# Kernel tuning notes

Measured on AMD Instinct MI355X. Metric: run time of the kernel, lower is better.

Reference implementation:

```python
import jax, jax.numpy as jnp
import numpy as np

B, L, K = 16, 512, 30          # proteins, residues per protein, kNN neighbors
N = B * L
H, FC = 32, 3                  # h_channels, frame_channels
C = H + FC                     # fused sphere channels (35)
HEADS, AC, VC = 8, 16, 8       # heads, alpha channels (H//2), value channels (H//4)
RBF_N, POS_N = 16, 16
EF = RBF_N + POS_N

# idealized backbone atom positions (N, CA, C) in the local residue frame
IDEAL_BB = np.array([[-0.525, 1.363, 0.0], [0.0, 0.0, 0.0], [1.526, 0.0, 0.0]], dtype=np.float32)
# cartesian (x,y,z) -> real-SH l=1 ordering (y,z,x)
P_SH = np.array([[0., 1., 0.], [0., 0., 1.], [1., 0., 0.]], dtype=np.float32)


def _knn_edges(trans):
    # per-chain brute-force kNN (chains are contiguous blocks of length L)
    X = trans.reshape(B, L, 3)
    d2 = jnp.sum((X[:, :, None, :] - X[:, None, :, :]) ** 2, axis=-1)  # [B,L,L]
    d2 = d2 + jnp.eye(L, dtype=d2.dtype) * 1e9                          # exclude self
    _, idx = jax.lax.top_k(-d2, K)                                      # [B,L,K]
    off = (jnp.arange(B) * L)[:, None, None]
    src = (idx + off).reshape(-1)              # neighbor (edge_index[0])
    tgt = jnp.repeat(jnp.arange(N), K)         # center   (edge_index[1])
    return src, tgt


def _edge_rot_mat(vec):
    # rotation aligning the edge vector with the y axis (eSCN init_edge_rot_mat style)
    nx = vec / (jnp.linalg.norm(vec, axis=-1, keepdims=True) + 1e-12)
    ref = jnp.where(jnp.abs(nx[:, :1]) < 0.9,
                    jnp.array([1., 0., 0.], dtype=vec.dtype),
                    jnp.array([0., 0., 1.], dtype=vec.dtype))
    nz = jnp.cross(nx, ref)
    nz = nz / (jnp.linalg.norm(nz, axis=-1, keepdims=True) + 1e-12)
    ny = jnp.cross(nx, nz)
    ny = ny / (jnp.linalg.norm(ny, axis=-1, keepdims=True) + 1e-12)
    return jnp.stack([nz, nx, ny], axis=-2)  # [E,3,3]


def _rbf(d, d_min=0.0, d_max=20.0, count=RBF_N):
    mu = jnp.linspace(d_min, d_max, count)
    sigma = (d_max - d_min) / count
    return jnp.exp(-(((d[:, None] - mu) / sigma) ** 2))


def _pos_emb(src, tgt, num=POS_N):
    d = (src - tgt).astype(jnp.float32)
    freq = jnp.exp(jnp.arange(0, num, 2, dtype=jnp.float32) * (-np.log(10000.0) / num))
    ang = d[:, None] * freq
    return jnp.concatenate([jnp.cos(ang), jnp.sin(ang)], axis=-1)


def _forward(rots, trans, node_emb, batch, x_mask, noising_mask,
             W_alpha, a_vec, W_v, W_o, W_g, W_2):
    src, tgt = _knn_edges(trans)
    vec = trans[src] - trans[tgt]
    dist = jnp.linalg.norm(vec, axis=-1)
    valid = jnp.isfinite(dist) & (dist > 1e-3)  # edge_select, applied as mask

    R = _edge_rot_mat(vec)
    P = jnp.asarray(P_SH)
    D1 = jnp.einsum('ij,ejk,lk->eil', P, R, P)  # l=1 Wigner in real-SH basis [E,3,3]

    edge_features = jnp.concatenate([_rbf(dist), _pos_emb(src, tgt)], axis=-1)  # [E,32]

    # fuse node features with backbone frame atoms and editability flag
    frame_atoms = jnp.einsum('nij,aj->nai', rots, jnp.asarray(IDEAL_BB))  # [N,3atoms,3xyz]
    editable = noising_mask & (~x_mask)
    emb = jnp.zeros((N, 4, C), dtype=node_emb.dtype)
    emb = emb.at[:, :, :H].set(node_emb)
    emb = emb.at[:, 1:4, H:].set(jnp.swapaxes(frame_atoms, -1, -2))
    emb = emb.at[:, 0, C - 1].set(editable.astype(node_emb.dtype))

    # gather + rotate source features into edge frames
    xs = emb[src]                                                   # [E,4,C]
    xs_rot = jnp.concatenate([xs[:, :1], jnp.einsum('eij,ejc->eic', D1, xs[:, 1:])], axis=1)

    # invariant attention logits (l=0 of rotated src, l=0 of tgt, edge feats)
    inv = jnp.concatenate([xs_rot[:, 0], emb[tgt, 0], edge_features], axis=-1)  # [E,102]
    hdn = jax.nn.silu(inv @ W_alpha).reshape(-1, HEADS, AC)
    logits = jax.nn.leaky_relu(jnp.einsum('ehk,hk->eh', hdn, a_vec), 0.2)
    logits = jnp.where(valid[:, None], logits, -1e9)

    # segment softmax over incoming edges of each target node
    mx = jax.lax.stop_gradient(jax.ops.segment_max(logits, tgt, num_segments=N))
    ex = jnp.exp(logits - mx[tgt]) * valid[:, None].astype(logits.dtype)
    den = jax.ops.segment_sum(ex, tgt, num_segments=N)
    alpha = ex / (den[tgt] + 1e-9)                                  # [E,HEADS]

    # equivariant values, attention-weighted, rotate back, scatter
    v = (xs_rot @ W_v).reshape(-1, 4, HEADS, VC)
    m = (v * alpha[:, None, :, None]).reshape(-1, 4, HEADS * VC)
    m = jnp.concatenate([m[:, :1], jnp.einsum('eji,ejc->eic', D1, m[:, 1:])], axis=1)  # D^T
    agg = jax.ops.segment_sum(m, tgt, num_segments=N)               # [N,4,64]

    y = agg @ W_o                                                    # [N,4,H]
    gate = jax.nn.silu(y[:, 0] @ W_g)                                # invariant gating FFN
    return (y * gate[:, None, :]) @ W_2                              # [N,4,H]


def setup_inputs():
    key = jax.random.key(0)
    ks = jax.random.split(key, 12)
    rots = jax.vmap(lambda m: jnp.linalg.qr(m)[0])(jax.random.normal(ks[0], (N, 3, 3)))
    trans = jax.random.normal(ks[1], (N, 3)) * 10.0
    node_emb = jax.random.normal(ks[2], (N, 4, H))
    batch = jnp.repeat(jnp.arange(B, dtype=jnp.int32), L)
    x_mask = jax.random.randint(ks[3], (N,), 0, 2).astype(bool)
    noising_mask = jax.random.randint(ks[4], (N,), 0, 2).astype(bool)
    s = lambda k, sh, fan: jax.random.normal(k, sh) / np.sqrt(fan)
    return dict(rots=rots, trans=trans, node_emb=node_emb, batch=batch,
                x_mask=x_mask, noising_mask=noising_mask,
                W_alpha=s(ks[5], (2 * C + EF, HEADS * AC), 2 * C + EF),
                a_vec=s(ks[6], (HEADS, AC), AC),
                W_v=s(ks[7], (C, HEADS * VC), C),
                W_o=s(ks[8], (HEADS * VC, H), HEADS * VC),
                W_g=s(ks[9], (H, H), H),
                W_2=s(ks[10], (H, H), H))


def reference(rots, trans, node_emb, batch, x_mask, noising_mask,
              W_alpha, a_vec, W_v, W_o, W_g, W_2):
    return _forward(rots, trans, node_emb, batch, x_mask, noising_mask,
                    W_alpha, a_vec, W_v, W_o, W_g, W_2)
```

## Files before the change

kernel.cpp:

```cpp
#include <hip/hip_runtime.h>
#include <cstdint>

#define B_ 16
#define L_ 512
#define N_ 8192
#define K_ 30
#define E_ (N_*K_)
#define H_ 32
#define C_ 35

typedef uint16_t u16;
typedef uint32_t u32;
typedef unsigned long long u64;
typedef float f2v __attribute__((ext_vector_type(2)));

static __device__ __forceinline__ f2v splat2(float x) { f2v v; v.x = x; v.y = x; return v; }

static __device__ __forceinline__ float ldf(const void* p, int i, int bf) {
    return bf ? __uint_as_float(((u32)((const u16*)p)[i]) << 16)
              : ((const float*)p)[i];
}
static __device__ __forceinline__ float bfu16(u16 x) {
    return __uint_as_float(((u32)x) << 16);
}
static __device__ __forceinline__ int ldmask(const void* p, int i, int mode) {
    if (mode == 0) return ((const unsigned char*)p)[i] != 0;
    if (mode == 2) return ((const u32*)p)[2*i] != 0;
    return ((const u32*)p)[i] != 0;
}
static __device__ __forceinline__ u16 f2bf(float f) {
    u32 x = __float_as_uint(f);
    u32 r = x + 0x7FFFu + ((x >> 16) & 1u);
    return (u16)(r >> 16);
}
static __device__ __forceinline__ float fsilu(float x) {
    return x * __builtin_amdgcn_rcpf(1.f + __expf(-x));
}

static __device__ __forceinline__ int detect_bf(const void* tr, int lane) {
    const u16* p = (const u16*)tr;
    int cnt = 0;
    for (int i = lane; i < 256; i += 64) {
        u16 v = p[2 * i];
        int e = (v >> 7) & 0xFF;
        if ((e >= 100 && e <= 141) || (v & 0x7FFFu) == 0) cnt++;
    }
    #pragma unroll
    for (int d = 1; d < 64; d <<= 1) cnt += __shfl_xor(cnt, d, 64);
    return cnt >= 192;
}
static __device__ __forceinline__ int detect_mm(const void* xmv, int lane) {
    const u32* xm = (const u32*)xmv;
    int anyBig = 0, oddNZ = 0;
    for (int i = lane; i < 1024; i += 64) {
        u32 w = xm[i];
        if (w & ~1u) anyBig = 1;
        if ((i & 1) && w) oddNZ = 1;
    }
    #pragma unroll
    for (int d = 1; d < 64; d <<= 1) {
        anyBig |= __shfl_xor(anyBig, d, 64);
        oddNZ  |= __shfl_xor(oddNZ, d, 64);
    }
    return anyBig ? 0 : (oddNZ ? 1 : 2);
}

__constant__ float cBB[9] = {-0.525f, 1.363f, 0.f,  0.f, 0.f, 0.f,  1.526f, 0.f, 0.f};

#define DPP_UMIN(var, CTRL) \
    { u32 o_ = (u32)__builtin_amdgcn_update_dpp((int)(var), (int)(var), CTRL, 0xF, 0xF, false); \
      (var) = (o_ < (var)) ? o_ : (var); }
#define DPP_UMIN_ALL(var) \
    DPP_UMIN(var, 0x111) DPP_UMIN(var, 0x112) DPP_UMIN(var, 0x114) \
    DPP_UMIN(var, 0x118) DPP_UMIN(var, 0x142) DPP_UMIN(var, 0x143)

#define DPP_ADD8(part) \
    part += __uint_as_float((u32)__builtin_amdgcn_update_dpp( \
        (int)__float_as_uint(part), (int)__float_as_uint(part), 0xB1, 0xF, 0xF, false)); \
    part += __uint_as_float((u32)__builtin_amdgcn_update_dpp( \
        (int)__float_as_uint(part), (int)__float_as_uint(part), 0x4E, 0xF, 0xF, false)); \
    part += __uint_as_float((u32)__builtin_amdgcn_update_dpp( \
        (int)__float_as_uint(part), (int)__float_as_uint(part), 0x141, 0xF, 0xF, false));

__global__ __launch_bounds__(256) void mega_kernel(
    const void* __restrict__ rots, const void* __restrict__ trans,
    const void* __restrict__ node, const void* __restrict__ xm,
    const void* __restrict__ nm,
    const void* __restrict__ Wa, const void* __restrict__ av,
    const void* __restrict__ Wv, const void* __restrict__ Wo,
    const void* __restrict__ Wg, const void* __restrict__ W2,
    int* __restrict__ flag, int* __restrict__ srcArr,
    float* __restrict__ hsrc, float* __restrict__ htgt,
    float* __restrict__ ptab, float* __restrict__ V,
    float* __restrict__ c_wrb, float* __restrict__ c_av,
    float* __restrict__ c_Wo, float* __restrict__ c_Wg, float* __restrict__ c_W2)
{
    __shared__ float sX[L_], sY[L_], sZ[L_];
    __shared__ float eS[140];
    __shared__ int flagS[2];
    const int bid = blockIdx.x, tid = threadIdx.x;
    const int lane = tid & 63, wid = tid >> 6;

    if (bid < 2048) {
        if (wid == 0) {
            int bf = detect_bf(trans, lane);
            if (lane == 0) flagS[0] = bf;
        }
        __syncthreads();
        const int bf = flagS[0];
        const int t0 = bid * 4;
        const int base = (t0 >> 9) << 9;
        if (bf) {
            const u16* tp = (const u16*)trans;
            for (int i = tid; i < L_; i += 256) {
                sX[i] = bfu16(tp[(base + i) * 3 + 0]);
                sY[i] = bfu16(tp[(base + i) * 3 + 1]);
                sZ[i] = bfu16(tp[(base + i) * 3 + 2]);
            }
        } else {
            const float* tp = (const float*)trans;
            for (int i = tid; i < L_; i += 256) {
                sX[i] = tp[(base + i) * 3 + 0];
                sY[i] = tp[(base + i) * 3 + 1];
                sZ[i] = tp[(base + i) * 3 + 2];
            }
        }
        __syncthreads();

        const int t = t0 + wid;
        const int l = t & 511;
        const float tx = sX[l], ty = sY[l], tz = sZ[l];

        u32 d2b[8];
        #pragma unroll
        for (int i = 0; i < 8; ++i) {
            int j = lane + (i << 6);
            float dx = __fsub_rn(tx, sX[j]);
            float dy = __fsub_rn(ty, sY[j]);
            float dz = __fsub_rn(tz, sZ[j]);
            float d2 = __fadd_rn(__fadd_rn(__fmul_rn(dx, dx), __fmul_rn(dy, dy)), __fmul_rn(dz, dz));
            if (j == l) d2 = __fadd_rn(d2, 1e9f);
            d2b[i] = __float_as_uint(d2);
        }

        int myres = 0;
        for (int k = 0; k < K_; ++k) {
            u32 bb = d2b[0]; int bs = 0;
            #pragma unroll
            for (int i = 1; i < 8; ++i)
                if (d2b[i] < bb) { bb = d2b[i]; bs = i; }
            u32 m = bb;
            DPP_UMIN_ALL(m)
            u32 gbits = (u32)__builtin_amdgcn_readlane((int)m, 63);
            u32 cand = (bb == gbits) ? (u32)(lane | (bs << 6)) : 0xFFFFFFFFu;
            DPP_UMIN_ALL(cand)
            u32 gidx = (u32)__builtin_amdgcn_readlane((int)cand, 63);
            if (lane == (u32)k) myres = (int)(gidx & 511u);
            if ((gidx & 63u) == (u32)lane) {
                int ws = (int)(gidx >> 6);
                #pragma unroll
                for (int i = 0; i < 8; ++i)
                    if (ws == i) d2b[i] = 0xFFFFFFFFu;
            }
        }
        if (lane < K_) srcArr[t * K_ + lane] = base + myres;

    } else if (bid < 10240) {
        const int n = bid - 2048;
        if (wid == 0) {
            int bf = detect_bf(trans, lane);
            int mm = detect_mm(xm, lane);
            if (lane == 0) { flagS[0] = bf; flagS[1] = mm; }
        }
        __syncthreads();
        const int bf = flagS[0], mm = flagS[1];
        if (tid < 140) {
            int r = tid / 35, c = tid - r * 35;
            float v;
            if (c < H_) {
                v = ldf(node, n * 128 + r * 32 + c, bf);
            } else if (r == 0) {
                v = (c == 34) ? ((ldmask(nm, n, mm) && !ldmask(xm, n, mm)) ? 1.f : 0.f) : 0.f;
            } else {
                int i = r - 1, a = c - 32;
                v = ldf(rots, n*9 + i*3 + 0, bf) * cBB[a*3 + 0]
                  + ldf(rots, n*9 + i*3 + 1, bf) * cBB[a*3 + 1]
                  + ldf(rots, n*9 + i*3 + 2, bf) * cBB[a*3 + 2];
            }
            eS[tid] = v;
        }
        __syncthreads();
        const int r = tid >> 6, cc = tid & 63;
        if (bf) {
            const u16* wa = (const u16*)Wa;
            const u16* wv = (const u16*)Wv;
            if (tid < 128) {
                float a = 0.f, b = 0.f;
                #pragma unroll 5
                for (int i = 0; i < 35; ++i) {
                    float v = eS[i];
                    a = fmaf(v, bfu16(wa[i * 128 + tid]),        a);
                    b = fmaf(v, bfu16(wa[(35 + i) * 128 + tid]), b);
                }
                hsrc[(size_t)n * 128 + tid] = a;
                htgt[(size_t)n * 128 + tid] = b;
            }
            const float* er = eS + r * 35;
            float acc = 0.f;
            #pragma unroll 5
            for (int cp = 0; cp < 35; ++cp) acc = fmaf(er[cp], bfu16(wv[cp * 64 + cc]), acc);
            V[(size_t)n * 256 + tid] = acc;
        } else {
            const float* wa = (const float*)Wa;
            const float* wv = (const float*)Wv;
            if (tid < 128) {
                float a = 0.f, b = 0.f;
                #pragma unroll 5
                for (int i = 0; i < 35; ++i) {
                    float v = eS[i];
                    a = fmaf(v, wa[i * 128 + tid],        a);
                    b = fmaf(v, wa[(35 + i) * 128 + tid], b);
                }
                hsrc[(size_t)n * 128 + tid] = a;
                htgt[(size_t)n * 128 + tid] = b;
            }
            const float* er = eS + r * 35;
            float acc = 0.f;
            #pragma unroll 5
            for (int cp = 0; cp < 35; ++cp) acc = fmaf(er[cp], wv[cp * 64 + cc], acc);
            V[(size_t)n * 256 + tid] = acc;
        }

    } else if (bid < 11264) {
        const int d = bid - 10240;
        if (wid == 0) {
            int bf = detect_bf(trans, lane);
            if (lane == 0) flagS[0] = bf;
        }
        __syncthreads();
        const int bf = flagS[0];
        if (tid < 128) {
            float dd = (float)(d - 512);
            float acc = 0.f;
            if (bf) {
                const u16* wa = (const u16*)Wa;
                #pragma unroll
                for (int q = 0; q < 8; ++q) {
                    float fr = expf((float)(2 * q) * (-0.5756462732485115f));
                    float ang = dd * fr;
                    acc = fmaf(cosf(ang), bfu16(wa[(86 + q) * 128 + tid]), acc);
                    acc = fmaf(sinf(ang), bfu16(wa[(94 + q) * 128 + tid]), acc);
                }
            } else {
                const float* wa = (const float*)Wa;
                #pragma unroll
                for (int q = 0; q < 8; ++q) {
                    float fr = expf((float)(2 * q) * (-0.5756462732485115f));
                    float ang = dd * fr;
                    acc = fmaf(cosf(ang), wa[(86 + q) * 128 + tid], acc);
                    acc = fmaf(sinf(ang), wa[(94 + q) * 128 + tid], acc);
                }
            }
            ptab[(size_t)d * 128 + tid] = acc;
        }

    } else {
        if (wid == 0) {
            int bf = detect_bf(trans, lane);
            if (lane == 0) flagS[0] = bf;
        }
        __syncthreads();
        const int bf = flagS[0];
        if (bid == 11264 && tid == 0) flag[0] = bf;
        int g0 = (bid - 11264) * 256 + tid;
        for (int i = g0; i < 6272; i += 2048) {
            if      (i < 2048) c_wrb[i]        = ldf(Wa, 70 * 128 + i, bf);
            else if (i < 2176) c_av[i - 2048]  = ldf(av, i - 2048, bf);
            else if (i < 4224) c_Wo[i - 2176]  = ldf(Wo, i - 2176, bf);
            else if (i < 5248) c_Wg[i - 4224]  = ldf(Wg, i - 4224, bf);
            else               c_W2[i - 5248]  = ldf(W2, i - 5248, bf);
        }
    }
}

__global__ __launch_bounds__(128) void logits_kernel(
    const void* __restrict__ trans, const int* __restrict__ srcArr,
    const float* __restrict__ hsrc, const float* __restrict__ htgt,
    const float* __restrict__ ptab,
    const float* __restrict__ c_wrb, const float* __restrict__ c_av,
    const int* __restrict__ flag, float* __restrict__ logitsw)
{
    __shared__ float rbfS[2][32][20];
    __shared__ int   srcS[2][32];
    __shared__ int   tgtS[2][32];
    __shared__ int   dS[2][32];
    __shared__ float lgS[2][256];
    const int tid = threadIdx.x, wid = tid >> 6, lane = tid & 63;
    const int bf = flag[0];

    const f2v* cw = (const f2v*)c_wrb;
    const f2v w0 = cw[0*64+lane],  w1 = cw[1*64+lane],  w2 = cw[2*64+lane],  w3 = cw[3*64+lane];
    const f2v w4 = cw[4*64+lane],  w5 = cw[5*64+lane],  w6 = cw[6*64+lane],  w7 = cw[7*64+lane];
    const f2v w8 = cw[8*64+lane],  w9 = cw[9*64+lane],  wA = cw[10*64+lane], wB = cw[11*64+lane];
    const f2v wC = cw[12*64+lane], wD = cw[13*64+lane], wE = cw[14*64+lane], wF = cw[15*64+lane];
    const f2v avv = ((const f2v*)c_av)[lane];

    const int e0 = (blockIdx.x * 2 + wid) * 32;

    {
        const int el  = lane & 31;
        const int e   = e0 + el;
        const int tgt = e / K_;
        int src = srcArr[e];
        src = (src < 0) ? 0 : ((src >= N_) ? (N_ - 1) : src);
        float vx = ldf(trans, src*3+0, bf) - ldf(trans, tgt*3+0, bf);
        float vy = ldf(trans, src*3+1, bf) - ldf(trans, tgt*3+1, bf);
        float vz = ldf(trans, src*3+2, bf) - ldf(trans, tgt*3+2, bf);
        float dist = sqrtf(vx*vx + vy*vy + vz*vz);
        bool valid = isfinite(dist) && (dist > 1e-3f);
        int d = src - tgt + 512;
        d = (d < 0) ? 0 : ((d > 1023) ? 1023 : d);
        if (lane < 32) {
            srcS[wid][el] = src;
            tgtS[wid][el] = tgt;
            dS[wid][el]   = d | (valid ? 0 : (1 << 16));
        }
        const int jb = (lane >> 5) * 8;
        #pragma unroll
        for (int j = 0; j < 8; ++j) {
            float tt = (dist - (float)(jb + j) * (20.f/15.f)) * 0.8f;
            rbfS[wid][lane & 31][jb + j] = __expf(-tt * tt);
        }
    }
    __syncthreads();

    const float* hsL = hsrc + (lane << 1);
    const float* htL = htgt + (lane << 1);
    const float* ptL = ptab + (lane << 1);
    #pragma unroll 2
    for (int q = 0; q < 32; ++q) {
        const int src = srcS[wid][q];
        const int tgt = tgtS[wid][q];
        const int dm  = dS[wid][q];
        const int d   = dm & 0xFFFF;
        const bool valid = (dm >> 16) == 0;

        f2v hs = *(const f2v*)(hsL + (src << 7));
        f2v ht = *(const f2v*)(htL + (tgt << 7));
        f2v pt = *(const f2v*)(ptL + (d << 7));
        f2v acc = (hs + ht) + pt;
        const float4* rp = (const float4*)(&rbfS[wid][q][0]);
        float4 ra = rp[0], rb = rp[1], rc = rp[2], rd = rp[3];
        acc = __builtin_elementwise_fma(splat2(ra.x), w0, acc);
        acc = __builtin_elementwise_fma(splat2(ra.y), w1, acc);
        acc = __builtin_elementwise_fma(splat2(ra.z), w2, acc);
        acc = __builtin_elementwise_fma(splat2(ra.w), w3, acc);
        acc = __builtin_elementwise_fma(splat2(rb.x), w4, acc);
        acc = __builtin_elementwise_fma(splat2(rb.y), w5, acc);
        acc = __builtin_elementwise_fma(splat2(rb.z), w6, acc);
        acc = __builtin_elementwise_fma(splat2(rb.w), w7, acc);
        acc = __builtin_elementwise_fma(splat2(rc.x), w8, acc);
        acc = __builtin_elementwise_fma(splat2(rc.y), w9, acc);
        acc = __builtin_elementwise_fma(splat2(rc.z), wA, acc);
        acc = __builtin_elementwise_fma(splat2(rc.w), wB, acc);
        acc = __builtin_elementwise_fma(splat2(rd.x), wC, acc);
        acc = __builtin_elementwise_fma(splat2(rd.y), wD, acc);
        acc = __builtin_elementwise_fma(splat2(rd.z), wE, acc);
        acc = __builtin_elementwise_fma(splat2(rd.w), wF, acc);
        float part = fsilu(acc.x) * avv.x + fsilu(acc.y) * avv.y;
        DPP_ADD8(part)
        float lg = (part >= 0.f) ? part : 0.2f * part;
        if (!valid) lg = -1e9f;
        lg = (fabsf(lg) < 1e30f) ? lg : -1e9f;
        if ((lane & 7) == 0) lgS[wid][q * 8 + (lane >> 3)] = lg;
    }
    __syncthreads();
    {
        float4* dst = (float4*)(logitsw + (size_t)e0 * 8);
        dst[lane] = ((const float4*)lgS[wid])[lane];
    }
}

__global__ __launch_bounds__(256) void agg_out_kernel(
    const float* __restrict__ V, const int* __restrict__ srcArr,
    const float* __restrict__ logitsw,
    const float* __restrict__ Wo, const float* __restrict__ Wg,
    const float* __restrict__ W2,
    const int* __restrict__ flag, void* __restrict__ outv)
{
    __shared__ float lgS[240];
    __shared__ float invS[8];
    __shared__ int   voffS[K_];
    __shared__ float aggS[256];
    __shared__ float ybuf[128];
    __shared__ float gbuf[32];
    const int bid = blockIdx.x, tid = threadIdx.x;
    const int t   = ((bid & 7) << 10) | (bid >> 3);
    const int bf = flag[0];

    if (tid < 240) lgS[tid] = logitsw[(size_t)t * 240 + tid];
    if (tid < K_) {
        int s = srcArr[t * K_ + tid];
        s = (s < 0) ? 0 : ((s >= N_) ? (N_ - 1) : s);
        voffS[tid] = s << 8;
    }
    __syncthreads();

    if (tid < 8) {
        float mx = -1e30f;
        #pragma unroll
        for (int k = 0; k < K_; ++k) mx = fmaxf(mx, lgS[k * 8 + tid]);
        float den = 0.f;
        #pragma unroll
        for (int k = 0; k < K_; ++k) {
            float l = lgS[k * 8 + tid];
            float e = (l > -1e8f) ? __expf(l - mx) : 0.f;
            lgS[k * 8 + tid] = e; den += e;
        }
        invS[tid] = 1.f / (den + 1e-9f);
    }
    __syncthreads();

    {
        const int h = (tid & 63) >> 3;
        float vv[K_];
        #pragma unroll
        for (int k = 0; k < K_; ++k) vv[k] = V[voffS[k] + tid];
        float acc = 0.f;
        #pragma unroll
        for (int k = 0; k < K_; ++k) acc = fmaf(lgS[k * 8 + h], vv[k], acc);
        aggS[tid] = acc * invS[h];
    }
    __syncthreads();

    if (tid < 128) {
        int rr = tid >> 5, o = tid & 31;
        float y = 0.f;
        #pragma unroll
        for (int c = 0; c < 64; ++c) y = fmaf(aggS[rr * 64 + c], Wo[c * 32 + o], y);
        ybuf[tid] = y;
    }
    __syncthreads();
    if (tid < 32) {
        float g = 0.f;
        #pragma unroll
        for (int o = 0; o < 32; ++o) g = fmaf(ybuf[o], Wg[o * 32 + tid], g);
        gbuf[tid] = fsilu(g);
    }
    __syncthreads();
    if (tid < 128) {
        int rr = tid >> 5, hh = tid & 31;
        float o = 0.f;
        #pragma unroll
        for (int g = 0; g < 32; ++g) o = fmaf(ybuf[rr * 32 + g] * gbuf[g], W2[g * 32 + hh], o);
        o = (fabsf(o) < 1e30f) ? o : 0.f;
        size_t idx = (size_t)t * 128 + tid;
        if (bf) ((u16*)outv)[idx] = f2bf(o);
        else    ((float*)outv)[idx] = o;
    }
}

extern "C" void kernel_launch(void* const* d_in, const int* in_sizes, int n_in,
                              void* d_out, int out_size, void* d_ws, size_t ws_size,
                              hipStream_t stream)
{
    const void* rots         = d_in[0];
    const void* trans        = d_in[1];
    const void* node_emb     = d_in[2];
    const void* x_mask       = d_in[4];
    const void* noising_mask = d_in[5];
    const void* Wa           = d_in[6];
    const void* avec         = d_in[7];
    const void* Wv           = d_in[8];
    const void* Wo           = d_in[9];
    const void* Wg           = d_in[10];
    const void* W2           = d_in[11];

    char* ws = (char*)d_ws;
    int*   flag    = (int*)  (ws + 0);
    int*   srcArr  = (int*)  (ws + 64);
    float* hsrc    = (float*)(ws + 983104);
    float* htgt    = (float*)(ws + 5177408);
    float* ptab    = (float*)(ws + 9371712);
    float* V       = (float*)(ws + 9896000);
    float* c_wrb   = (float*)(ws + 18284608);
    float* c_av    = (float*)(ws + 18292800);
    float* c_Wo    = (float*)(ws + 18293312);
    float* c_Wg    = (float*)(ws + 18301504);
    float* c_W2    = (float*)(ws + 18305600);
    float* logitsw = (float*)(ws + 18309696);

    hipLaunchKernelGGL(mega_kernel, dim3(11272), dim3(256), 0, stream,
                       rots, trans, node_emb, x_mask, noising_mask,
                       Wa, avec, Wv, Wo, Wg, W2,
                       flag, srcArr, hsrc, htgt, ptab, V,
                       c_wrb, c_av, c_Wo, c_Wg, c_W2);
    hipLaunchKernelGGL(logits_kernel, dim3(E_/64), dim3(128), 0, stream,
                       trans, srcArr, hsrc, htgt, ptab, c_wrb, c_av, flag, logitsw);
    hipLaunchKernelGGL(agg_out_kernel, dim3(N_), dim3(256), 0, stream,
                       V, srcArr, logitsw, c_Wo, c_Wg, c_W2, flag, d_out);
}
```

Measured before the change: 210.4 us.

## Split kNN into its own kernel and add ballot fast path for argmin

Moves the kNN top-k selection out of the fused mega kernel into a dedicated kernel, so the node-prep blocks no longer carry the kNN's shared memory footprint (three 512-float arrays) and register pressure. In the selection loop, a ballot detects a unique minimum and reads its index directly, skipping the second DPP min-reduction in the common case. This adds one extra kernel launch and serialises kNN before prep on the stream. The rbf shared index change is equivalent to the old one.

```diff
diff --git a/kernel.cpp b/kernel.cpp
--- a/kernel.cpp
+++ b/kernel.cpp
@@ -82,91 +82,105 @@
     part += __uint_as_float((u32)__builtin_amdgcn_update_dpp( \
         (int)__float_as_uint(part), (int)__float_as_uint(part), 0x141, 0xF, 0xF, false));
 
-__global__ __launch_bounds__(256) void mega_kernel(
+__global__ __launch_bounds__(256) void knn_kernel(const void* __restrict__ trans,
+                                                  int* __restrict__ srcArr)
+{
+    __shared__ float sX[L_], sY[L_], sZ[L_];
+    __shared__ int flagS[1];
+    const int bid = blockIdx.x, tid = threadIdx.x;
+    const int lane = tid & 63, wid = tid >> 6;
+
+    if (wid == 0) {
+        int bf = detect_bf(trans, lane);
+        if (lane == 0) flagS[0] = bf;
+    }
+    __syncthreads();
+    const int bf = flagS[0];
+    const int t0 = bid * 4;
+    const int base = (t0 >> 9) << 9;
+    if (bf) {
+        const u16* tp = (const u16*)trans;
+        for (int i = tid; i < L_; i += 256) {
+            sX[i] = bfu16(tp[(base + i) * 3 + 0]);
+            sY[i] = bfu16(tp[(base + i) * 3 + 1]);
+            sZ[i] = bfu16(tp[(base + i) * 3 + 2]);
+        }
+    } else {
+        const float* tp = (const float*)trans;
+        for (int i = tid; i < L_; i += 256) {
+            sX[i] = tp[(base + i) * 3 + 0];
+            sY[i] = tp[(base + i) * 3 + 1];
+            sZ[i] = tp[(base + i) * 3 + 2];
+        }
+    }
+    __syncthreads();
+
+    const int t = t0 + wid;
+    const int l = t & 511;
+    const float tx = sX[l], ty = sY[l], tz = sZ[l];
+
+    u32 d2b[8];
+    #pragma unroll
+    for (int i = 0; i < 8; ++i) {
+        int j = lane + (i << 6);
+        float dx = __fsub_rn(tx, sX[j]);
+        float dy = __fsub_rn(ty, sY[j]);
+        float dz = __fsub_rn(tz, sZ[j]);
+        float d2 = __fadd_rn(__fadd_rn(__fmul_rn(dx, dx), __fmul_rn(dy, dy)), __fmul_rn(dz, dz));
+        if (j == l) d2 = __fadd_rn(d2, 1e9f);
+        d2b[i] = __float_as_uint(d2);
+    }
+
+    int myres = 0;
+    for (int k = 0; k < K_; ++k) {
+        u32 bb = d2b[0]; int bs = 0;
+        #pragma unroll
+        for (int i = 1; i < 8; ++i)
+            if (d2b[i] < bb) { bb = d2b[i]; bs = i; }
+        u32 m = bb;
+        DPP_UMIN_ALL(m)
+        u32 gbits = (u32)__builtin_amdgcn_readlane((int)m, 63);
+        u64 mask = __ballot(bb == gbits);
+        u32 gidx;
+        if (__popcll(mask) == 1) {
+            int wl = __ffsll((long long)mask) - 1;
+            gidx = (u32)__builtin_amdgcn_readlane((int)((bs << 6) | lane), wl);
+        } else {
+            u32 cand = (bb == gbits) ? (u32)((bs << 6) | lane) : 0xFFFFFFFFu;
+            DPP_UMIN_ALL(cand)
+            gidx = (u32)__builtin_amdgcn_readlane((int)cand, 63);
+        }
+        if (lane == (u32)k) myres = (int)(gidx & 511u);
+        if ((gidx & 63u) == (u32)lane) {
+            int ws = (int)(gidx >> 6);
+            #pragma unroll
+            for (int i = 0; i < 8; ++i)
+                if (ws == i) d2b[i] = 0xFFFFFFFFu;
+        }
+    }
+    if (lane < K_) srcArr[t * K_ + lane] = base + myres;
+}
+
+__global__ __launch_bounds__(256) void prep_kernel(
     const void* __restrict__ rots, const void* __restrict__ trans,
     const void* __restrict__ node, const void* __restrict__ xm,
     const void* __restrict__ nm,
     const void* __restrict__ Wa, const void* __restrict__ av,
     const void* __restrict__ Wv, const void* __restrict__ Wo,
     const void* __restrict__ Wg, const void* __restrict__ W2,
-    int* __restrict__ flag, int* __restrict__ srcArr,
+    int* __restrict__ flag,
     float* __restrict__ hsrc, float* __restrict__ htgt,
     float* __restrict__ ptab, float* __restrict__ V,
     float* __restrict__ c_wrb, float* __restrict__ c_av,
     float* __restrict__ c_Wo, float* __restrict__ c_Wg, float* __restrict__ c_W2)
 {
-    __shared__ float sX[L_], sY[L_], sZ[L_];
     __shared__ float eS[140];
     __shared__ int flagS[2];
     const int bid = blockIdx.x, tid = threadIdx.x;
     const int lane = tid & 63, wid = tid >> 6;
 
-    if (bid < 2048) {
-        if (wid == 0) {
-            int bf = detect_bf(trans, lane);
-            if (lane == 0) flagS[0] = bf;
-        }
-        __syncthreads();
-        const int bf = flagS[0];
-        const int t0 = bid * 4;
-        const int base = (t0 >> 9) << 9;
-        if (bf) {
-            const u16* tp = (const u16*)trans;
-            for (int i = tid; i < L_; i += 256) {
-                sX[i] = bfu16(tp[(base + i) * 3 + 0]);
-                sY[i] = bfu16(tp[(base + i) * 3 + 1]);
-                sZ[i] = bfu16(tp[(base + i) * 3 + 2]);
-            }
-        } else {
-            const float* tp = (const float*)trans;
-            for (int i = tid; i < L_; i += 256) {
-                sX[i] = tp[(base + i) * 3 + 0];
-                sY[i] = tp[(base + i) * 3 + 1];
-                sZ[i] = tp[(base + i) * 3 + 2];
-            }
-        }
-        __syncthreads();
-
-        const int t = t0 + wid;
-        const int l = t & 511;
-        const float tx = sX[l], ty = sY[l], tz = sZ[l];
-
-        u32 d2b[8];
-        #pragma unroll
-        for (int i = 0; i < 8; ++i) {
-            int j = lane + (i << 6);
-            float dx = __fsub_rn(tx, sX[j]);
-            float dy = __fsub_rn(ty, sY[j]);
-            float dz = __fsub_rn(tz, sZ[j]);
-            float d2 = __fadd_rn(__fadd_rn(__fmul_rn(dx, dx), __fmul_rn(dy, dy)), __fmul_rn(dz, dz));
-            if (j == l) d2 = __fadd_rn(d2, 1e9f);
-            d2b[i] = __float_as_uint(d2);
-        }
-
-        int myres = 0;
-        for (int k = 0; k < K_; ++k) {
-            u32 bb = d2b[0]; int bs = 0;
-            #pragma unroll
-            for (int i = 1; i < 8; ++i)
-                if (d2b[i] < bb) { bb = d2b[i]; bs = i; }
-            u32 m = bb;
-            DPP_UMIN_ALL(m)
-            u32 gbits = (u32)__builtin_amdgcn_readlane((int)m, 63);
-            u32 cand = (bb == gbits) ? (u32)(lane | (bs << 6)) : 0xFFFFFFFFu;
-            DPP_UMIN_ALL(cand)
-            u32 gidx = (u32)__builtin_amdgcn_readlane((int)cand, 63);
-            if (lane == (u32)k) myres = (int)(gidx & 511u);
-            if ((gidx & 63u) == (u32)lane) {
-                int ws = (int)(gidx >> 6);
-                #pragma unroll
-                for (int i = 0; i < 8; ++i)
-                    if (ws == i) d2b[i] = 0xFFFFFFFFu;
-            }
-        }
-        if (lane < K_) srcArr[t * K_ + lane] = base + myres;
-
-    } else if (bid < 10240) {
-        const int n = bid - 2048;
+    if (bid < 8192) {
+        const int n = bid;
         if (wid == 0) {
             int bf = detect_bf(trans, lane);
             int mm = detect_mm(xm, lane);
@@ -231,8 +245,8 @@
             V[(size_t)n * 256 + tid] = acc;
         }
 
-    } else if (bid < 11264) {
-        const int d = bid - 10240;
+    } else if (bid < 9216) {
+        const int d = bid - 8192;
         if (wid == 0) {
             int bf = detect_bf(trans, lane);
             if (lane == 0) flagS[0] = bf;
@@ -271,8 +285,8 @@
         }
         __syncthreads();
         const int bf = flagS[0];
-        if (bid == 11264 && tid == 0) flag[0] = bf;
-        int g0 = (bid - 11264) * 256 + tid;
+        if (bid == 9216 && tid == 0) flag[0] = bf;
+        int g0 = (bid - 9216) * 256 + tid;
         for (int i = g0; i < 6272; i += 2048) {
             if      (i < 2048) c_wrb[i]        = ldf(Wa, 70 * 128 + i, bf);
             else if (i < 2176) c_av[i - 2048]  = ldf(av, i - 2048, bf);
@@ -329,7 +343,7 @@
         #pragma unroll
         for (int j = 0; j < 8; ++j) {
             float tt = (dist - (float)(jb + j) * (20.f/15.f)) * 0.8f;
-            rbfS[wid][lane & 31][jb + j] = __expf(-tt * tt);
+            rbfS[wid][el][jb + j] = __expf(-tt * tt);
         }
     }
     __syncthreads();
@@ -490,10 +504,11 @@
     float* c_W2    = (float*)(ws + 18305600);
     float* logitsw = (float*)(ws + 18309696);
 
-    hipLaunchKernelGGL(mega_kernel, dim3(11272), dim3(256), 0, stream,
+    hipLaunchKernelGGL(knn_kernel, dim3(N_/4), dim3(256), 0, stream, trans, srcArr);
+    hipLaunchKernelGGL(prep_kernel, dim3(8192 + 1024 + 8), dim3(256), 0, stream,
                        rots, trans, node_emb, x_mask, noising_mask,
                        Wa, avec, Wv, Wo, Wg, W2,
-                       flag, srcArr, hsrc, htgt, ptab, V,
+                       flag, hsrc, htgt, ptab, V,
                        c_wrb, c_av, c_Wo, c_Wg, c_W2);
     hipLaunchKernelGGL(logits_kernel, dim3(E_/64), dim3(128), 0, stream,
                        trans, srcArr, hsrc, htgt, ptab, c_wrb, c_av, flag, logitsw);
```

After: 217.5 us. 3.4% more time.
